# Performance work log

Hardware: AMD Instinct MI355X
Metric: run time of the kernel (lower is better)

Reference implementation:

```python
import jax, jax.numpy as jnp
import numpy as np


def setup_inputs() -> dict:
    key = jax.random.key(0)
    kq, kk, kv, km = jax.random.split(key, 4)
    B, H, S, D = 2, 16, 2048, 64
    queries = jax.random.normal(kq, (B, H, S, D), dtype=jnp.float32)
    keys = jax.random.normal(kk, (B, H, S, D), dtype=jnp.float32)
    values = jax.random.normal(kv, (B, H, S, D), dtype=jnp.float32)
    # additive binary mask (1 = masked position), broadcast over batch/heads
    mask = jax.random.randint(km, (1, 1, S, S), 0, 2, dtype=jnp.int32)
    return {"queries": queries, "keys": keys, "values": values,
            "mask": mask, "key_dim": D}


def reference(queries, keys, values, mask, key_dim):
    # scores = Q K^T / sqrt(d)   -> [B, H, S, S]
    scale = 1.0 / jnp.sqrt(jnp.asarray(key_dim, dtype=jnp.float32))
    scores = jnp.einsum('bhqd,bhkd->bhqk', queries, keys) * scale
    # additive mask: masked positions get -1e9
    scores = scores + (-1.0e9) * mask.astype(scores.dtype)
    weights = jax.nn.softmax(scores, axis=-1)
    # attention output: weights @ V -> [B, H, S, D]
    return jnp.einsum('bhqk,bhkd->bhqd', weights, values)
```

## Files before the change

kernel.cpp:

```cpp
#include <hip/hip_runtime.h>

typedef __attribute__((ext_vector_type(8))) short short8;
typedef __attribute__((ext_vector_type(4))) float floatx4;
typedef __attribute__((ext_vector_type(2))) unsigned int uint2v;

#define S_LEN 2048
#define D_HEAD 64
#define NT64 (S_LEN / 64)
#define PITCH 72
#define TP 73
#define SCALE2 0.18033688f
#define MASK_BIAS2 -2.0e9f

static __device__ __forceinline__ unsigned short f2bf(float f) {
  unsigned int x = __builtin_bit_cast(unsigned int, f);
  x += 0x7fffu + ((x >> 16) & 1u);
  return (unsigned short)(x >> 16);
}
static __device__ __forceinline__ float bf2f(unsigned short u) {
  unsigned int x = ((unsigned int)u) << 16;
  return __builtin_bit_cast(float, x);
}
static __device__ __forceinline__ short8 cvt8(const float* __restrict__ p) {
  float4 a = *(const float4*)p;
  float4 b = *(const float4*)(p + 4);
  short8 r;
  r[0] = (short)f2bf(a.x); r[1] = (short)f2bf(a.y);
  r[2] = (short)f2bf(a.z); r[3] = (short)f2bf(a.w);
  r[4] = (short)f2bf(b.x); r[5] = (short)f2bf(b.y);
  r[6] = (short)f2bf(b.z); r[7] = (short)f2bf(b.w);
  return r;
}
static __device__ __forceinline__ short8 cvt8s(const float* __restrict__ p) {
  float4 a = *(const float4*)p;
  float4 b = *(const float4*)(p + 4);
  short8 r;
  r[0] = (short)f2bf(a.x * SCALE2); r[1] = (short)f2bf(a.y * SCALE2);
  r[2] = (short)f2bf(a.z * SCALE2); r[3] = (short)f2bf(a.w * SCALE2);
  r[4] = (short)f2bf(b.x * SCALE2); r[5] = (short)f2bf(b.y * SCALE2);
  r[6] = (short)f2bf(b.z * SCALE2); r[7] = (short)f2bf(b.w * SCALE2);
  return r;
}
static __device__ __forceinline__ void cp16(const void* g, void* l) {
  __builtin_amdgcn_global_load_lds(
      (const __attribute__((address_space(1))) unsigned int*)g,
      (__attribute__((address_space(3))) unsigned int*)l, 16, 0, 0);
}
static __device__ __forceinline__ unsigned int pk2f(float a, float b) {
  const unsigned int ab = __builtin_bit_cast(unsigned int, a) + 0x8000u;
  const unsigned int bb = __builtin_bit_cast(unsigned int, b) + 0x8000u;
  return __builtin_amdgcn_perm(bb, ab, 0x07060302u);
}
static __device__ __forceinline__ void plswap32(unsigned int& a, unsigned int& b) {
#if __has_builtin(__builtin_amdgcn_permlane32_swap)
  uint2v r = __builtin_amdgcn_permlane32_swap(a, b, false, false);
  a = r[0]; b = r[1];
#else
  asm volatile("v_permlane32_swap_b32 %0, %1" : "+v"(a), "+v"(b));
#endif
}
static __device__ __forceinline__ void plswap16(unsigned int& a, unsigned int& b) {
#if __has_builtin(__builtin_amdgcn_permlane16_swap)
  uint2v r = __builtin_amdgcn_permlane16_swap(a, b, false, false);
  a = r[0]; b = r[1];
#else
  asm volatile("v_permlane16_swap_b32 %0, %1" : "+v"(a), "+v"(b));
#endif
}

__global__ __launch_bounds__(256) void prep(
    const float* __restrict__ K, const float* __restrict__ V,
    const int* __restrict__ mask,
    unsigned short* __restrict__ Kws, unsigned short* __restrict__ Vws,
    unsigned long long* __restrict__ Mb, int BH)
{
  __shared__ unsigned short t[D_HEAD * TP];
  const int tid = threadIdx.x;
  const int nbK = BH * 64;
  const int nbV = BH * 32;
  int b = blockIdx.x;

  if (b < nbK) {
    const int tt   = b * 256 + tid;
    const int bh   = tt >> 14;
    const int rem  = tt & 16383;
    const int tile = rem >> 9;
    const int n    = rem & 511;
    const int row  = n >> 3;
    const int col8 = (n & 7) ^ (row & 7);
    short8 r = cvt8(K + ((size_t)(bh * S_LEN + tile * 64 + row)) * D_HEAD + col8 * 8);
    *(short8*)(Kws + (size_t)tt * 8) = r;
    return;
  }
  b -= nbK;
  if (b < nbV) {
    const int tile = b & 31;
    const int bh   = b >> 5;
    const int s0   = tile * 64;
    const float* Vb = V + (size_t)bh * S_LEN * D_HEAD;
#pragma unroll
    for (int p = 0; p < 4; ++p) {
      const int s  = p * 16 + (tid >> 4);
      const int d0 = (tid & 15) * 4;
      float4 v = *(const float4*)(Vb + (size_t)(s0 + s) * D_HEAD + d0);
      unsigned short* dst = &t[s * TP + d0];
      dst[0] = f2bf(v.x); dst[1] = f2bf(v.y); dst[2] = f2bf(v.z); dst[3] = f2bf(v.w);
    }
    __syncthreads();
    unsigned short* Vo = Vws + ((size_t)(bh * 32 + tile)) * 4096;
#pragma unroll
    for (int p = 0; p < 2; ++p) {
      const int n    = p * 256 + tid;
      const int d    = n >> 3;
      const int col8 = (n & 7) ^ (d & 7);
      short8 r;
#pragma unroll
      for (int j = 0; j < 8; ++j) r[j] = (short)t[(col8 * 8 + j) * TP + d];
      *(short8*)(Vo + (size_t)n * 8) = r;
    }
    return;
  }
  b -= nbV;
  const int rg   = b >> 2;
  const int cq   = b & 3;
  const int lane = tid & 63;
  const int row  = rg * 4 + (tid >> 6);
#pragma unroll 8
  for (int c = cq * 8; c < cq * 8 + 8; ++c) {
    const int mv = mask[(size_t)row * S_LEN + c * 64 + lane];
    const unsigned long long bm = __ballot(mv != 0);
    if (lane == 0) Mb[(size_t)row * NT64 + c] = bm;
  }
}

__global__ __launch_bounds__(256, 2) void fa_fwd9(
    const float* __restrict__ Q,
    const unsigned short* __restrict__ Kws,
    const unsigned short* __restrict__ Vws,
    const unsigned long long* __restrict__ Mb,
    float* __restrict__ Out)
{
  __shared__ unsigned short Kbuf[3][64 * 64];
  __shared__ unsigned short Vbuf[3][64 * 64];

  const int tid  = threadIdx.x;
  const int wv   = tid >> 6;
  const int lane = tid & 63;
  const int quad = lane >> 4;
  const int l16  = lane & 15;
  const int l8   = l16 & 7;

  const int nwg  = gridDim.x;
  const int flat = blockIdx.x;
  const int swz  = (flat & 7) * (nwg >> 3) + (flat >> 3);
  const int bh   = swz >> 4;
  const int qw   = (swz & 15) * 128 + wv * 32;

  const float* Qb = Q + (size_t)bh * S_LEN * D_HEAD;
  const unsigned short* KT = Kws + (size_t)bh * NT64 * 4096;
  const unsigned short* VT = Vws + (size_t)bh * NT64 * 4096;

  auto stage = [&](int kt, int buf) {
#pragma unroll
    for (int j = 0; j < 2; ++j) {
      const int c0 = (wv * 2 + j) * 64;
      cp16(KT + (size_t)kt * 4096 + (size_t)(c0 + lane) * 8, &Kbuf[buf][c0 * 8]);
      cp16(VT + (size_t)kt * 4096 + (size_t)(c0 + lane) * 8, &Vbuf[buf][c0 * 8]);
    }
  };

  stage(0, 0);
  stage(1, 1);

  short8 qfrag[2][2];
#pragma unroll
  for (int g = 0; g < 2; ++g)
#pragma unroll
    for (int w = 0; w < 2; ++w)
      qfrag[g][w] = cvt8s(Qb + (size_t)(qw + g * 16 + l16) * D_HEAD + w * 32 + quad * 8);

  short8 kones;
#pragma unroll
  for (int j = 0; j < 8; ++j) kones[j] = (short)0x3F80;

  floatx4 ot[2][4];
#pragma unroll
  for (int g = 0; g < 2; ++g)
#pragma unroll
    for (int dt = 0; dt < 4; ++dt) ot[g][dt] = (floatx4){0.f, 0.f, 0.f, 0.f};
  floatx4 lacc[2];
  lacc[0] = (floatx4){0.f, 0.f, 0.f, 0.f};
  lacc[1] = (floatx4){0.f, 0.f, 0.f, 0.f};

  const unsigned long long* mrowp[2];
#pragma unroll
  for (int g = 0; g < 2; ++g)
    mrowp[g] = Mb + (size_t)(qw + g * 16 + l16) * NT64;

  floatx4 stA[2][4], stB[2][4];

  auto qk = [&](floatx4 (&sdst)[2][4], const unsigned short* Kl) {
#pragma unroll
    for (int g = 0; g < 2; ++g)
#pragma unroll
      for (int nt = 0; nt < 4; ++nt) sdst[g][nt] = (floatx4){0.f, 0.f, 0.f, 0.f};
    __builtin_amdgcn_s_setprio(1);
#pragma unroll
    for (int w = 0; w < 2; ++w)
#pragma unroll
      for (int nt = 0; nt < 4; ++nt) {
        short8 kf = *(const short8*)&Kl[(nt * 16 + l16) * 64 + (((w * 4 + quad) ^ l8) * 8)];
        sdst[0][nt] = __builtin_amdgcn_mfma_f32_16x16x32_bf16(kf, qfrag[0][w], sdst[0][nt], 0, 0, 0);
        sdst[1][nt] = __builtin_amdgcn_mfma_f32_16x16x32_bf16(kf, qfrag[1][w], sdst[1][nt], 0, 0, 0);
      }
    __builtin_amdgcn_s_setprio(0);
  };

  auto sm_pv = [&](floatx4 (&scur)[2][4], const int kt, const unsigned short* Vl) {
    short8 pf[2][2];
#pragma unroll
    for (int g = 0; g < 2; ++g) {
      const unsigned long long mw = mrowp[g][kt];
      unsigned int Wk[4][2];
#pragma unroll
      for (int nt = 0; nt < 4; ++nt) {
        const unsigned nib = (unsigned)(mw >> (nt * 16 + quad * 4)) & 0xFu;
        float p[4];
#pragma unroll
        for (int r = 0; r < 4; ++r) {
          float pv = __builtin_amdgcn_exp2f(scur[g][nt][r]);
          p[r] = ((nib >> r) & 1u) ? 0.0f : pv;
        }
        Wk[nt][0] = pk2f(p[0], p[1]);
        Wk[nt][1] = pk2f(p[2], p[3]);
      }
#pragma unroll
      for (int w = 0; w < 2; ++w) {
        unsigned a0 = Wk[2 * w][0], b0 = Wk[2 * w + 1][0];
        plswap32(a0, b0);
        plswap16(a0, b0);
        unsigned a1 = Wk[2 * w][1], b1 = Wk[2 * w + 1][1];
        plswap32(a1, b1);
        plswap16(a1, b1);
        uint4 wd;
        wd.x = a0; wd.y = a1; wd.z = b0; wd.w = b1;
        pf[g][w] = __builtin_bit_cast(short8, wd);
      }
    }
    __builtin_amdgcn_s_setprio(1);
#pragma unroll
    for (int w = 0; w < 2; ++w) {
      lacc[0] = __builtin_amdgcn_mfma_f32_16x16x32_bf16(kones, pf[0][w], lacc[0], 0, 0, 0);
      lacc[1] = __builtin_amdgcn_mfma_f32_16x16x32_bf16(kones, pf[1][w], lacc[1], 0, 0, 0);
#pragma unroll
      for (int dt = 0; dt < 4; ++dt) {
        short8 vf = *(const short8*)&Vl[(dt * 16 + l16) * 64 + (((w * 4 + quad) ^ l8) * 8)];
        ot[0][dt] = __builtin_amdgcn_mfma_f32_16x16x32_bf16(vf, pf[0][w], ot[0][dt], 0, 0, 0);
        ot[1][dt] = __builtin_amdgcn_mfma_f32_16x16x32_bf16(vf, pf[1][w], ot[1][dt], 0, 0, 0);
      }
    }
    __builtin_amdgcn_s_setprio(0);
  };

  auto body = [&](floatx4 (&scur)[2][4], floatx4 (&snxt)[2][4],
                  const int kt, const int bV, const int bKn, const int bS) {
    asm volatile("s_waitcnt vmcnt(0)" ::: "memory");
    __builtin_amdgcn_s_barrier();
    if (kt + 2 < NT64) stage(kt + 2, bS);
    qk(snxt, Kbuf[bKn]);
    sm_pv(scur, kt, Vbuf[bV]);
  };

  asm volatile("s_waitcnt vmcnt(0)" ::: "memory");
  __builtin_amdgcn_s_barrier();
  qk(stA, Kbuf[0]);

  int bV = 0, bKn = 1, bS = 2;
  for (int kt = 0; kt < NT64 - 2; kt += 2) {
    body(stA, stB, kt, bV, bKn, bS);
    { const int t = bV; bV = bKn; bKn = bS; bS = t; }
    body(stB, stA, kt + 1, bV, bKn, bS);
    { const int t = bV; bV = bKn; bKn = bS; bS = t; }
  }
  body(stA, stB, NT64 - 2, bV, bKn, bS);
  { const int t = bV; bV = bKn; bKn = bS; bS = t; }
  sm_pv(stB, NT64 - 1, Vbuf[bV]);

#pragma unroll
  for (int g = 0; g < 2; ++g) {
    const float invl = 1.0f / lacc[g][0];
    float* Ob = Out + (size_t)bh * S_LEN * D_HEAD + (size_t)(qw + g * 16 + l16) * D_HEAD;
#pragma unroll
    for (int dt = 0; dt < 4; ++dt) {
      float4 v;
      v.x = ot[g][dt][0] * invl; v.y = ot[g][dt][1] * invl;
      v.z = ot[g][dt][2] * invl; v.w = ot[g][dt][3] * invl;
      *(float4*)(Ob + dt * 16 + quad * 4) = v;
    }
  }
}

__global__ __launch_bounds__(256) void fa_fwd(
    const float* __restrict__ Q, const float* __restrict__ K, const float* __restrict__ V,
    const int* __restrict__ mask, float* __restrict__ Out)
{
  __shared__ unsigned short Vt[D_HEAD * PITCH];
  __shared__ unsigned short Plds[4][16 * PITCH];
  const int tid = threadIdx.x, wv = tid >> 6, lane = tid & 63, quad = lane >> 4, l16 = lane & 15;
  const int bh = blockIdx.y, qw = blockIdx.x * 64 + wv * 16;
  const float* Qb = Q + (size_t)bh * S_LEN * D_HEAD;
  const float* Kb = K + (size_t)bh * S_LEN * D_HEAD;
  const float* Vb = V + (size_t)bh * S_LEN * D_HEAD;
  short8 qfrag[2];
#pragma unroll
  for (int w = 0; w < 2; ++w)
    qfrag[w] = cvt8(Qb + (size_t)(qw + l16) * D_HEAD + w * 32 + quad * 8);
  floatx4 o[4];
#pragma unroll
  for (int nt = 0; nt < 4; ++nt) o[nt] = (floatx4){0.f, 0.f, 0.f, 0.f};
  float m_run[4], l_run[4];
#pragma unroll
  for (int r = 0; r < 4; ++r) { m_run[r] = -1.0e30f; l_run[r] = 0.f; }
  unsigned short* pl = &Plds[wv][0];
  for (int kt = 0; kt < NT64; ++kt) {
    const int k0 = kt * 64;
    __syncthreads();
#pragma unroll
    for (int it = 0; it < 2; ++it) {
      const int s = it * 32 + (tid >> 3), d0 = (tid & 7) * 8, dblk = (tid & 7);
      const int swz = (((s >> 3) ^ dblk) & 7) * 8 + (s & 7);
      const float* vp = Vb + (size_t)(k0 + s) * D_HEAD + d0;
      float4 a = *(const float4*)vp; float4 bb = *(const float4*)(vp + 4);
      const float vvv[8] = {a.x, a.y, a.z, a.w, bb.x, bb.y, bb.z, bb.w};
#pragma unroll
      for (int j = 0; j < 8; ++j) Vt[(d0 + j) * PITCH + swz] = f2bf(vvv[j]);
    }
    __syncthreads();
    floatx4 scf[4];
#pragma unroll
    for (int nt = 0; nt < 4; ++nt) scf[nt] = (floatx4){0.f, 0.f, 0.f, 0.f};
#pragma unroll
    for (int w = 0; w < 2; ++w)
#pragma unroll
      for (int nt = 0; nt < 4; ++nt) {
        short8 kf = cvt8(Kb + (size_t)(k0 + nt * 16 + l16) * D_HEAD + w * 32 + quad * 8);
        scf[nt] = __builtin_amdgcn_mfma_f32_16x16x32_bf16(qfrag[w], kf, scf[nt], 0, 0, 0);
      }
    float s_val[4][4], mloc[4] = {-1.0e30f, -1.0e30f, -1.0e30f, -1.0e30f};
#pragma unroll
    for (int nt = 0; nt < 4; ++nt)
#pragma unroll
      for (int r = 0; r < 4; ++r) {
        const int mk = mask[(size_t)(qw + quad * 4 + r) * S_LEN + (k0 + nt * 16 + l16)];
        const float sv = scf[nt][r] * SCALE2 + (mk ? MASK_BIAS2 : 0.0f);
        s_val[nt][r] = sv; mloc[r] = fmaxf(mloc[r], sv);
      }
#pragma unroll
    for (int r = 0; r < 4; ++r)
#pragma unroll
      for (int off = 1; off < 16; off <<= 1) mloc[r] = fmaxf(mloc[r], __shfl_xor(mloc[r], off));
    float alpha[4], rsum[4];
#pragma unroll
    for (int r = 0; r < 4; ++r) {
      const float mnew = fmaxf(m_run[r], mloc[r]);
      alpha[r] = exp2f(m_run[r] - mnew); m_run[r] = mnew; rsum[r] = 0.f;
    }
#pragma unroll
    for (int nt = 0; nt < 4; ++nt)
#pragma unroll
      for (int r = 0; r < 4; ++r) {
        const float p = exp2f(s_val[nt][r] - m_run[r]);
        const unsigned short ph = f2bf(p);
        rsum[r] += bf2f(ph);
        pl[(quad * 4 + r) * PITCH + nt * 16 + l16] = ph;
      }
    __syncthreads();
#pragma unroll
    for (int r = 0; r < 4; ++r) {
#pragma unroll
      for (int off = 1; off < 16; off <<= 1) rsum[r] += __shfl_xor(rsum[r], off);
      l_run[r] = l_run[r] * alpha[r] + rsum[r];
    }
#pragma unroll
    for (int nt = 0; nt < 4; ++nt)
#pragma unroll
      for (int r = 0; r < 4; ++r) o[nt][r] *= alpha[r];
#pragma unroll
    for (int w = 0; w < 2; ++w) {
      short8 af = *(const short8*)&pl[l16 * PITCH + w * 32 + quad * 8];
#pragma unroll
      for (int nt = 0; nt < 4; ++nt) {
        const int d = nt * 16 + l16, blk = ((w * 4 + quad) ^ (d >> 3)) & 7;
        short8 vf = *(const short8*)&Vt[d * PITCH + blk * 8];
        o[nt] = __builtin_amdgcn_mfma_f32_16x16x32_bf16(af, vf, o[nt], 0, 0, 0);
      }
    }
  }
  float invl[4];
#pragma unroll
  for (int r = 0; r < 4; ++r) invl[r] = 1.0f / l_run[r];
  float* Ob = Out + (size_t)bh * S_LEN * D_HEAD;
#pragma unroll
  for (int nt = 0; nt < 4; ++nt)
#pragma unroll
    for (int r = 0; r < 4; ++r)
      Ob[(size_t)(qw + quad * 4 + r) * D_HEAD + nt * 16 + l16] = o[nt][r] * invl[r];
}

extern "C" void kernel_launch(void* const* d_in, const int* in_sizes, int n_in,
                              void* d_out, int out_size, void* d_ws, size_t ws_size,
                              hipStream_t stream) {
  const float* Q = (const float*)d_in[0];
  const float* K = (const float*)d_in[1];
  const float* V = (const float*)d_in[2];
  const int* mask = (const int*)d_in[3];
  float* Out = (float*)d_out;
  const int BH = in_sizes[0] / (S_LEN * D_HEAD);
  const size_t NH = (size_t)BH * S_LEN * D_HEAD;
  const size_t nMb = (size_t)S_LEN * NT64;
  const size_t need = NH * 2 * 2 + nMb * 8;

  if (ws_size >= need) {
    unsigned short* Kws = (unsigned short*)d_ws;
    unsigned short* Vws = Kws + NH;
    unsigned long long* Mbits = (unsigned long long*)(Vws + NH);
    const int nbPrep = BH * 64 + BH * 32 + S_LEN;
    prep<<<dim3(nbPrep), 256, 0, stream>>>(K, V, mask, Kws, Vws, Mbits, BH);
    fa_fwd9<<<dim3((S_LEN / 128) * BH), 256, 0, stream>>>(Q, Kws, Vws, Mbits, Out);
  } else {
    fa_fwd<<<dim3(S_LEN / 64, BH), 256, 0, stream>>>(Q, K, V, mask, Out);
  }
}
```

Measured before the change: 170.2 us.

## Shrink per-wave query tile to 16 rows and use double buffering for occupancy

Each wave now handles 16 query rows instead of 32, and each workgroup covers 64 query rows instead of 128. This doubles the grid to 1024 blocks and raises the launch-bounds occupancy target from 2 to 4. The triple-buffered, software-pipelined QK/softmax-PV schedule is replaced by a simple double-buffered loop that syncs with __syncthreads each tile. The aim is to hide latency through more resident waves and fewer registers rather than through explicit intra-wave pipelining. In exchange, K/V tiles are reused across fewer query rows, so LDS and global traffic per FLOP doubles, and the QK and PV phases no longer overlap within a wave.

```diff
diff --git a/kernel.cpp b/kernel.cpp
--- a/kernel.cpp
+++ b/kernel.cpp
@@ -133,15 +133,15 @@
   }
 }
 
-__global__ __launch_bounds__(256, 2) void fa_fwd9(
+__global__ __launch_bounds__(256, 4) void fa_fwd10(
     const float* __restrict__ Q,
     const unsigned short* __restrict__ Kws,
     const unsigned short* __restrict__ Vws,
     const unsigned long long* __restrict__ Mb,
     float* __restrict__ Out)
 {
-  __shared__ unsigned short Kbuf[3][64 * 64];
-  __shared__ unsigned short Vbuf[3][64 * 64];
+  __shared__ unsigned short Kbuf[2][64 * 64];
+  __shared__ unsigned short Vbuf[2][64 * 64];
 
   const int tid  = threadIdx.x;
   const int wv   = tid >> 6;
@@ -153,8 +153,8 @@
   const int nwg  = gridDim.x;
   const int flat = blockIdx.x;
   const int swz  = (flat & 7) * (nwg >> 3) + (flat >> 3);
-  const int bh   = swz >> 4;
-  const int qw   = (swz & 15) * 128 + wv * 32;
+  const int bh   = swz >> 5;
+  const int qw   = (swz & 31) * 64 + wv * 16;
 
   const float* Qb = Q + (size_t)bh * S_LEN * D_HEAD;
   const unsigned short* KT = Kws + (size_t)bh * NT64 * 4096;
@@ -170,133 +170,95 @@
   };
 
   stage(0, 0);
-  stage(1, 1);
-
-  short8 qfrag[2][2];
-#pragma unroll
-  for (int g = 0; g < 2; ++g)
-#pragma unroll
-    for (int w = 0; w < 2; ++w)
-      qfrag[g][w] = cvt8s(Qb + (size_t)(qw + g * 16 + l16) * D_HEAD + w * 32 + quad * 8);
+
+  short8 qfrag[2];
+#pragma unroll
+  for (int w = 0; w < 2; ++w)
+    qfrag[w] = cvt8s(Qb + (size_t)(qw + l16) * D_HEAD + w * 32 + quad * 8);
 
   short8 kones;
 #pragma unroll
   for (int j = 0; j < 8; ++j) kones[j] = (short)0x3F80;
 
-  floatx4 ot[2][4];
-#pragma unroll
-  for (int g = 0; g < 2; ++g)
-#pragma unroll
-    for (int dt = 0; dt < 4; ++dt) ot[g][dt] = (floatx4){0.f, 0.f, 0.f, 0.f};
-  floatx4 lacc[2];
-  lacc[0] = (floatx4){0.f, 0.f, 0.f, 0.f};
-  lacc[1] = (floatx4){0.f, 0.f, 0.f, 0.f};
-
-  const unsigned long long* mrowp[2];
-#pragma unroll
-  for (int g = 0; g < 2; ++g)
-    mrowp[g] = Mb + (size_t)(qw + g * 16 + l16) * NT64;
-
-  floatx4 stA[2][4], stB[2][4];
-
-  auto qk = [&](floatx4 (&sdst)[2][4], const unsigned short* Kl) {
-#pragma unroll
-    for (int g = 0; g < 2; ++g)
-#pragma unroll
-      for (int nt = 0; nt < 4; ++nt) sdst[g][nt] = (floatx4){0.f, 0.f, 0.f, 0.f};
+  floatx4 ot[4];
+#pragma unroll
+  for (int dt = 0; dt < 4; ++dt) ot[dt] = (floatx4){0.f, 0.f, 0.f, 0.f};
+  floatx4 lacc = (floatx4){0.f, 0.f, 0.f, 0.f};
+
+  const unsigned long long* mrow = Mb + (size_t)(qw + l16) * NT64;
+
+  __syncthreads();
+
+  for (int kt = 0; kt < NT64; ++kt) {
+    const int cur = kt & 1;
+    if (kt + 1 < NT64) stage(kt + 1, cur ^ 1);
+    const unsigned short* Kl = Kbuf[cur];
+    const unsigned short* Vl = Vbuf[cur];
+
+    floatx4 st[4];
+#pragma unroll
+    for (int nt = 0; nt < 4; ++nt) st[nt] = (floatx4){0.f, 0.f, 0.f, 0.f};
     __builtin_amdgcn_s_setprio(1);
 #pragma unroll
     for (int w = 0; w < 2; ++w)
 #pragma unroll
       for (int nt = 0; nt < 4; ++nt) {
         short8 kf = *(const short8*)&Kl[(nt * 16 + l16) * 64 + (((w * 4 + quad) ^ l8) * 8)];
-        sdst[0][nt] = __builtin_amdgcn_mfma_f32_16x16x32_bf16(kf, qfrag[0][w], sdst[0][nt], 0, 0, 0);
-        sdst[1][nt] = __builtin_amdgcn_mfma_f32_16x16x32_bf16(kf, qfrag[1][w], sdst[1][nt], 0, 0, 0);
+        st[nt] = __builtin_amdgcn_mfma_f32_16x16x32_bf16(kf, qfrag[w], st[nt], 0, 0, 0);
       }
     __builtin_amdgcn_s_setprio(0);
-  };
-
-  auto sm_pv = [&](floatx4 (&scur)[2][4], const int kt, const unsigned short* Vl) {
-    short8 pf[2][2];
-#pragma unroll
-    for (int g = 0; g < 2; ++g) {
-      const unsigned long long mw = mrowp[g][kt];
-      unsigned int Wk[4][2];
-#pragma unroll
-      for (int nt = 0; nt < 4; ++nt) {
-        const unsigned nib = (unsigned)(mw >> (nt * 16 + quad * 4)) & 0xFu;
-        float p[4];
-#pragma unroll
-        for (int r = 0; r < 4; ++r) {
-          float pv = __builtin_amdgcn_exp2f(scur[g][nt][r]);
-          p[r] = ((nib >> r) & 1u) ? 0.0f : pv;
-        }
-        Wk[nt][0] = pk2f(p[0], p[1]);
-        Wk[nt][1] = pk2f(p[2], p[3]);
-      }
-#pragma unroll
-      for (int w = 0; w < 2; ++w) {
-        unsigned a0 = Wk[2 * w][0], b0 = Wk[2 * w + 1][0];
-        plswap32(a0, b0);
-        plswap16(a0, b0);
-        unsigned a1 = Wk[2 * w][1], b1 = Wk[2 * w + 1][1];
-        plswap32(a1, b1);
-        plswap16(a1, b1);
-        uint4 wd;
-        wd.x = a0; wd.y = a1; wd.z = b0; wd.w = b1;
-        pf[g][w] = __builtin_bit_cast(short8, wd);
-      }
-    }
+
+    const unsigned long long mw = mrow[kt];
+    unsigned int Wk[4][2];
+#pragma unroll
+    for (int nt = 0; nt < 4; ++nt) {
+      const unsigned nib = (unsigned)(mw >> (nt * 16 + quad * 4)) & 0xFu;
+      float p[4];
+#pragma unroll
+      for (int r = 0; r < 4; ++r) {
+        float pv = __builtin_amdgcn_exp2f(st[nt][r]);
+        p[r] = ((nib >> r) & 1u) ? 0.0f : pv;
+      }
+      Wk[nt][0] = pk2f(p[0], p[1]);
+      Wk[nt][1] = pk2f(p[2], p[3]);
+    }
+    short8 pf[2];
+#pragma unroll
+    for (int w = 0; w < 2; ++w) {
+      unsigned a0 = Wk[2 * w][0], b0 = Wk[2 * w + 1][0];
+      plswap32(a0, b0);
+      plswap16(a0, b0);
+      unsigned a1 = Wk[2 * w][1], b1 = Wk[2 * w + 1][1];
+      plswap32(a1, b1);
+      plswap16(a1, b1);
+      uint4 wd;
+      wd.x = a0; wd.y = a1; wd.z = b0; wd.w = b1;
+      pf[w] = __builtin_bit_cast(short8, wd);
+    }
+
     __builtin_amdgcn_s_setprio(1);
 #pragma unroll
     for (int w = 0; w < 2; ++w) {
-      lacc[0] = __builtin_amdgcn_mfma_f32_16x16x32_bf16(kones, pf[0][w], lacc[0], 0, 0, 0);
-      lacc[1] = __builtin_amdgcn_mfma_f32_16x16x32_bf16(kones, pf[1][w], lacc[1], 0, 0, 0);
+      lacc = __builtin_amdgcn_mfma_f32_16x16x32_bf16(kones, pf[w], lacc, 0, 0, 0);
 #pragma unroll
       for (int dt = 0; dt < 4; ++dt) {
         short8 vf = *(const short8*)&Vl[(dt * 16 + l16) * 64 + (((w * 4 + quad) ^ l8) * 8)];
-        ot[0][dt] = __builtin_amdgcn_mfma_f32_16x16x32_bf16(vf, pf[0][w], ot[0][dt], 0, 0, 0);
-        ot[1][dt] = __builtin_amdgcn_mfma_f32_16x16x32_bf16(vf, pf[1][w], ot[1][dt], 0, 0, 0);
+        ot[dt] = __builtin_amdgcn_mfma_f32_16x16x32_bf16(vf, pf[w], ot[dt], 0, 0, 0);
       }
     }
     __builtin_amdgcn_s_setprio(0);
-  };
-
-  auto body = [&](floatx4 (&scur)[2][4], floatx4 (&snxt)[2][4],
-                  const int kt, const int bV, const int bKn, const int bS) {
-    asm volatile("s_waitcnt vmcnt(0)" ::: "memory");
-    __builtin_amdgcn_s_barrier();
-    if (kt + 2 < NT64) stage(kt + 2, bS);
-    qk(snxt, Kbuf[bKn]);
-    sm_pv(scur, kt, Vbuf[bV]);
-  };
-
-  asm volatile("s_waitcnt vmcnt(0)" ::: "memory");
-  __builtin_amdgcn_s_barrier();
-  qk(stA, Kbuf[0]);
-
-  int bV = 0, bKn = 1, bS = 2;
-  for (int kt = 0; kt < NT64 - 2; kt += 2) {
-    body(stA, stB, kt, bV, bKn, bS);
-    { const int t = bV; bV = bKn; bKn = bS; bS = t; }
-    body(stB, stA, kt + 1, bV, bKn, bS);
-    { const int t = bV; bV = bKn; bKn = bS; bS = t; }
-  }
-  body(stA, stB, NT64 - 2, bV, bKn, bS);
-  { const int t = bV; bV = bKn; bKn = bS; bS = t; }
-  sm_pv(stB, NT64 - 1, Vbuf[bV]);
-
-#pragma unroll
-  for (int g = 0; g < 2; ++g) {
-    const float invl = 1.0f / lacc[g][0];
-    float* Ob = Out + (size_t)bh * S_LEN * D_HEAD + (size_t)(qw + g * 16 + l16) * D_HEAD;
-#pragma unroll
-    for (int dt = 0; dt < 4; ++dt) {
-      float4 v;
-      v.x = ot[g][dt][0] * invl; v.y = ot[g][dt][1] * invl;
-      v.z = ot[g][dt][2] * invl; v.w = ot[g][dt][3] * invl;
-      *(float4*)(Ob + dt * 16 + quad * 4) = v;
-    }
+
+    __syncthreads();
+  }
+
+  const float invl = 1.0f / lacc[0];
+  float* Ob = Out + (size_t)bh * S_LEN * D_HEAD + (size_t)(qw + l16) * D_HEAD;
+#pragma unroll
+  for (int dt = 0; dt < 4; ++dt) {
+    float4 v;
+    v.x = ot[dt][0] * invl; v.y = ot[dt][1] * invl;
+    v.z = ot[dt][2] * invl; v.w = ot[dt][3] * invl;
+    *(float4*)(Ob + dt * 16 + quad * 4) = v;
   }
 }
 
@@ -426,7 +388,7 @@
     unsigned long long* Mbits = (unsigned long long*)(Vws + NH);
     const int nbPrep = BH * 64 + BH * 32 + S_LEN;
     prep<<<dim3(nbPrep), 256, 0, stream>>>(K, V, mask, Kws, Vws, Mbits, BH);
-    fa_fwd9<<<dim3((S_LEN / 128) * BH), 256, 0, stream>>>(Q, Kws, Vws, Mbits, Out);
+    fa_fwd10<<<dim3((S_LEN / 64) * BH), 256, 0, stream>>>(Q, Kws, Vws, Mbits, Out);
   } else {
     fa_fwd<<<dim3(S_LEN / 64, BH), 256, 0, stream>>>(Q, K, V, mask, Out);
   }
```

New measurement: 162.9 us. -4.3%, faster.
